# Performance work log

Measured on AMD Instinct MI355X. Metric: run time of the kernel, lower is better.

Reference implementation:

```python
import jax, jax.numpy as jnp
import numpy as np

B, S, D = 8, 1024, 2048
H, HD = 16, 128          # n_heads, head_dim (H*HD == D)
ROPE = 64                # rotary dims per head (front slice)
MAXB, MAXS = 10, 1024    # kv-cache buffer sizes (hardcoded in module)
START_POS = 0


def _apply_rope(x, cos_half, sin_half):
    # x: (BH, S, ROPE); cos/sin_half: (S, ROPE//2) -> tiled to (S, ROPE)
    cos_full = jnp.concatenate([cos_half, cos_half], axis=-1)
    sin_full = jnp.concatenate([sin_half, sin_half], axis=-1)
    half = x.shape[-1] // 2
    x1, x2 = x[..., :half], x[..., half:]
    rotated = jnp.concatenate([-x2, x1], axis=-1)
    return x * cos_full + rotated * sin_full


def setup_inputs() -> dict:
    key = jax.random.key(0)
    ks = jax.random.split(key, 6)
    sc = 0.02
    x = jax.random.normal(ks[0], (B, S, D), dtype=jnp.float32)
    wq = jax.random.normal(ks[1], (D, D), dtype=jnp.float32) * sc
    wk = jax.random.normal(ks[2], (D, D), dtype=jnp.float32) * sc
    wv = jax.random.normal(ks[3], (D, D), dtype=jnp.float32) * sc
    wo = jax.random.normal(ks[4], (D, D), dtype=jnp.float32) * sc
    bq = jnp.zeros((D,), jnp.float32)
    bk = jnp.zeros((D,), jnp.float32)
    bv = jnp.zeros((D,), jnp.float32)
    bo = jnp.zeros((D,), jnp.float32)
    # RoPE tables (HF "half" layout): angles over positions
    half = ROPE // 2
    inv_freq = 1.0 / (10000.0 ** (jnp.arange(half, dtype=jnp.float32) / half))
    ang = jnp.arange(S, dtype=jnp.float32)[:, None] * inv_freq[None, :]  # (S, half)
    cos_half = jnp.cos(ang)
    sin_half = jnp.sin(ang)
    mask = jnp.zeros((S, S), jnp.float32)  # additive mask, (seq, end_pos)
    cache_k = jnp.zeros((MAXB, MAXS, H * HD), jnp.float32)
    cache_v = jnp.zeros((MAXB, MAXS, H * HD), jnp.float32)
    return {
        "x": x, "wq": wq, "bq": bq, "wk": wk, "bk": bk, "wv": wv, "bv": bv,
        "wo": wo, "bo": bo, "cos_half": cos_half, "sin_half": sin_half,
        "mask": mask, "cache_k": cache_k, "cache_v": cache_v,
        "start_pos": START_POS,
    }


def reference(x, wq, bq, wk, bk, wv, bv, wo, bo, cos_half, sin_half, mask,
              cache_k, cache_v, start_pos):
    b, s, _ = x.shape
    end_pos = start_pos + s
    # QKV projections (torch Linear: y = x @ W.T + b)
    q = (x @ wq.T + bq).reshape(b, s, H, HD)
    k = (x @ wk.T + bk).reshape(b, s, H, HD)
    v = (x @ wv.T + bv).reshape(b, s, H, HD)
    # Partial RoPE on the first ROPE dims of each head
    q_head = q[..., :ROPE].transpose(0, 2, 1, 3).reshape(b * H, s, ROPE)
    k_head = k[..., :ROPE].transpose(0, 2, 1, 3).reshape(b * H, s, ROPE)
    q_head = _apply_rope(q_head, cos_half, sin_half)
    k_head = _apply_rope(k_head, cos_half, sin_half)
    q_head = q_head.reshape(b, H, s, ROPE).transpose(0, 2, 1, 3)
    k_head = k_head.reshape(b, H, s, ROPE).transpose(0, 2, 1, 3)
    q = jnp.concatenate([q_head, q[..., ROPE:]], axis=-1)
    k = jnp.concatenate([k_head, k[..., ROPE:]], axis=-1)
    # KV-cache write then read (start_pos is a static python int)
    cache_k = jax.lax.dynamic_update_slice(cache_k, k.reshape(b, s, H * HD), (0, start_pos, 0))
    cache_v = jax.lax.dynamic_update_slice(cache_v, v.reshape(b, s, H * HD), (0, start_pos, 0))
    k_cached = cache_k[:b, :end_pos].reshape(b, end_pos, H, HD)
    v_cached = cache_v[:b, :end_pos].reshape(b, end_pos, H, HD)
    # Unnormalized attention: no softmax, no scaling
    scores = jnp.einsum('bshd,bthd->bsht', q, k_cached)  # (B,S,H,T)
    scores = scores + mask[:, None, :]                   # (S,1,T) broadcast
    a_sum = jnp.einsum('bsht,bthd->bshd', scores, v_cached)
    out = a_sum.reshape(b, s, H * HD) @ wo.T + bo
    return out
```

## Files before the change

### kernel.cpp

```cpp
#include <hip/hip_runtime.h>
#include <stdint.h>

#define B_ 8
#define S_ 1024
#define D_ 2048
#define H_ 16
#define HD_ 128
#define NROW 8192
#define NQKV 6144

typedef __bf16 bf16;
typedef bf16  bf16x8 __attribute__((ext_vector_type(8)));
typedef bf16  bf16x4 __attribute__((ext_vector_type(4)));
typedef float f32x4  __attribute__((ext_vector_type(4)));

#define AS1 __attribute__((address_space(1)))
#define AS3 __attribute__((address_space(3)))

__device__ __forceinline__ void gl_lds16(const bf16* g, bf16* l) {
  __builtin_amdgcn_global_load_lds((AS1 void*)g, (AS3 void*)l, 16, 0, 0);
}

__global__ __launch_bounds__(256) void prep(const float* __restrict__ x,
                                            const float* __restrict__ wq,
                                            const float* __restrict__ wk,
                                            const float* __restrict__ wv,
                                            const float* __restrict__ wo,
                                            const float* __restrict__ mask,
                                            const float* __restrict__ bq,
                                            const float* __restrict__ bk,
                                            const float* __restrict__ bv,
                                            bf16* __restrict__ xb,
                                            bf16* __restrict__ wqkvb,
                                            bf16* __restrict__ wob,
                                            bf16* __restrict__ maskb,
                                            float* __restrict__ bqkv) {
  long i = (long)blockIdx.x * 256 + threadIdx.x;
  if (i < 8650752) {
    const float* src; bf16* dst; long j;
    if (i < 4194304)      { src = x;    dst = xb;              j = i; }
    else if (i < 5242880) { src = wq;   dst = wqkvb;           j = i - 4194304; }
    else if (i < 6291456) { src = wk;   dst = wqkvb + 4194304; j = i - 5242880; }
    else if (i < 7340032) { src = wv;   dst = wqkvb + 8388608; j = i - 6291456; }
    else if (i < 8388608) { src = wo;   dst = wob;             j = i - 7340032; }
    else                  { src = mask; dst = maskb;           j = i - 8388608; }
    float4 v = reinterpret_cast<const float4*>(src)[j];
    bf16x4 o;
    o.x = (bf16)v.x; o.y = (bf16)v.y; o.z = (bf16)v.z; o.w = (bf16)v.w;
    reinterpret_cast<bf16x4*>(dst)[j] = o;
  } else {
    long e = (i - 8650752) * 4;
    const float* s = (e < 2048) ? bq + e : (e < 4096 ? bk + (e - 2048) : bv + (e - 4096));
    *reinterpret_cast<float4*>(bqkv + e) = *reinterpret_cast<const float4*>(s);
  }
}

#define READ_A4(QA, KS, Ab)                                                   \
  _Pragma("unroll") for (int mi = 0; mi < 4; mi++)                            \
    af[mi] = *reinterpret_cast<const bf16x8*>(                                \
        (Ab) + aoff + ((((QA)*4 + mi)*2) + (KS))*512);

#define READ_B4(KS, Bb)                                                       \
  _Pragma("unroll") for (int ni = 0; ni < 4; ni++)                            \
    bfr[ni] = *reinterpret_cast<const bf16x8*>(                               \
        (Bb) + boff + ((ni*2) + (KS))*512);

#define MFMA16(QA)                                                            \
  _Pragma("unroll") for (int mi = 0; mi < 4; mi++)                            \
  _Pragma("unroll") for (int ni = 0; ni < 4; ni++)                            \
    acc[(QA)*4 + mi][ni] = __builtin_amdgcn_mfma_f32_16x16x32_bf16(           \
        af[mi], bfr[ni], acc[(QA)*4 + mi][ni], 0, 0, 0);

#define STAGE_H0(An, Bn, koff)                                                \
  gl_lds16(agA + (koff),           (An) + wid*1024);                          \
  gl_lds16(agA + 128*la + (koff),  (An) + (wid + 8)*1024);                    \
  gl_lds16(agB + (koff),           (Bn) + wid*1024);                          \
  gl_lds16(agB + 128*lb + (koff),  (Bn) + (wid + 8)*1024);

#define STAGE_H1(An, Bn, koff)                                                \
  gl_lds16(agA + (koff) + 32,          (An) + wid*1024 + 512);                \
  gl_lds16(agA + 128*la + (koff) + 32, (An) + (wid + 8)*1024 + 512);          \
  gl_lds16(agB + (koff) + 32,          (Bn) + wid*1024 + 512);                \
  gl_lds16(agB + 128*lb + (koff) + 32, (Bn) + (wid + 8)*1024 + 512);

#define GEMM256_MAIN_LOOP(NT)                                                 \
  { bf16* An = lds; bf16* Bn = lds + 16384;                                   \
    STAGE_H0(An, Bn, 0); STAGE_H1(An, Bn, 0); }                               \
  for (int t = 0; t < (NT); ++t) {                                            \
    const bf16* Ab = lds + (t & 1) * 32768;                                   \
    const bf16* Bb = Ab + 16384;                                              \
    bf16* An = lds + ((t & 1) ^ 1) * 32768;                                   \
    bf16* Bn = An + 16384;                                                    \
    const long kn = (long)(t + 1) * 64;                                       \
    const bool pf = (t + 1) < (NT);                                           \
    bf16x8 af[4], bfr[4];                                                     \
    asm volatile("s_waitcnt vmcnt(4)" ::: "memory");                          \
    __builtin_amdgcn_s_barrier();                                             \
    READ_A4(0, 0, Ab); READ_B4(0, Bb);                                        \
    if (pf) { STAGE_H0(An, Bn, kn); }                                         \
    asm volatile("s_waitcnt lgkmcnt(0)" ::: "memory");                        \
    __builtin_amdgcn_sched_barrier(0);                                        \
    __builtin_amdgcn_s_setprio(1); MFMA16(0); __builtin_amdgcn_s_setprio(0);  \
    READ_A4(1, 0, Ab);                                                        \
    asm volatile("s_waitcnt lgkmcnt(0)" ::: "memory");                        \
    __builtin_amdgcn_sched_barrier(0);                                        \
    __builtin_amdgcn_s_setprio(1); MFMA16(1); __builtin_amdgcn_s_setprio(0);  \
    if (pf) asm volatile("s_waitcnt vmcnt(4)" ::: "memory");                  \
    else    asm volatile("s_waitcnt vmcnt(0)" ::: "memory");                  \
    __builtin_amdgcn_s_barrier();                                             \
    READ_A4(0, 1, Ab); READ_B4(1, Bb);                                        \
    if (pf) { STAGE_H1(An, Bn, kn); }                                         \
    asm volatile("s_waitcnt lgkmcnt(0)" ::: "memory");                        \
    __builtin_amdgcn_sched_barrier(0);                                        \
    __builtin_amdgcn_s_setprio(1); MFMA16(0); __builtin_amdgcn_s_setprio(0);  \
    READ_A4(1, 1, Ab);                                                        \
    asm volatile("s_waitcnt lgkmcnt(0)" ::: "memory");                        \
    __builtin_amdgcn_sched_barrier(0);                                        \
    __builtin_amdgcn_s_setprio(1); MFMA16(1); __builtin_amdgcn_s_setprio(0);  \
  }

template <typename CT, bool BIAS, bool ACCUM, bool ROPE>
__global__ __launch_bounds__(512, 2) void gemm256(const bf16* __restrict__ A,
                                                  const bf16* __restrict__ Bm,
                                                  const float* __restrict__ bias,
                                                  CT* __restrict__ C,
                                                  int M, int N, int K,
                                                  long la, long lb, long lc,
                                                  long za, long zb, long zc,
                                                  const float* __restrict__ chp,
                                                  const float* __restrict__ shp) {
  extern __shared__ __align__(16) bf16 lds[];
  const int z = blockIdx.z;
  A  += (long)z * za;
  Bm += (long)z * zb;
  C  += (long)z * zc;
  const int tid  = threadIdx.x;
  const int wid  = tid >> 6;
  const int lane = tid & 63;
  const int wm0 = (wid >> 2) * 128;
  const int wn0 = (wid & 3) * 64;
  const int m0 = blockIdx.y * 256, n0 = blockIdx.x * 256;

  const int rr = lane >> 2;
  const int cc = ((lane & 3) * 8) ^ ((rr & 8) << 1);
  const bf16* agA = A  + (long)(m0 + wid * 16 + rr) * la + cc;
  const bf16* agB = Bm + (long)(n0 + wid * 16 + rr) * lb + cc;

  const int swz  = ((lane >> 4) * 8) ^ ((lane & 8) << 1);
  const int aoff = (wm0 >> 4) * 1024 + (lane & 15) * 32 + swz;
  const int boff = (wn0 >> 4) * 1024 + (lane & 15) * 32 + swz;

  f32x4 acc[8][4] = {};
  const int NT = K >> 6;

  GEMM256_MAIN_LOOP(NT);

#pragma unroll
  for (int mi = 0; mi < 8; mi++) {
    float vals[4][4];
#pragma unroll
    for (int ni = 0; ni < 4; ni++) {
      const int col = n0 + wn0 + ni * 16 + (lane & 15);
      float bv = 0.0f;
      if constexpr (BIAS) bv = bias[col];
#pragma unroll
      for (int r = 0; r < 4; r++) vals[ni][r] = acc[mi][ni][r] + bv;
    }
    if constexpr (ROPE) {
      if ((n0 + wn0) < 4096 && (((n0 + wn0) & 127) == 0)) {
#pragma unroll
        for (int ni = 0; ni < 2; ni++)
#pragma unroll
          for (int r = 0; r < 4; r++) {
            const int srow = (m0 + wm0 + mi * 16 + (lane >> 4) * 4 + r) & (S_ - 1);
            const int hd = ni * 16 + (lane & 15);
            const float c  = chp[srow * 32 + hd];
            const float sn = shp[srow * 32 + hd];
            const float a  = vals[ni][r], b2 = vals[ni + 2][r];
            vals[ni][r]     = a * c - b2 * sn;
            vals[ni + 2][r] = b2 * c + a * sn;
          }
      }
    }
#pragma unroll
    for (int ni = 0; ni < 4; ni++) {
      const int col = n0 + wn0 + ni * 16 + (lane & 15);
      const long base = (long)(m0 + wm0 + mi * 16 + (lane >> 4) * 4) * lc + col;
#pragma unroll
      for (int r = 0; r < 4; r++) {
        float v = vals[ni][r];
        if constexpr (ACCUM) v += (float)C[base + (long)r * lc];
        C[base + (long)r * lc] = (CT)v;
      }
    }
  }
}

__global__ __launch_bounds__(512, 2) void pv256(const bf16* __restrict__ Am,
                                                const bf16* __restrict__ Vt,
                                                const bf16* __restrict__ QKV,
                                                const bf16* __restrict__ W2,
                                                bf16* __restrict__ Ob) {
  extern __shared__ __align__(16) bf16 lds[];
  const int z = blockIdx.z;
  const bf16* A  = Am;
  const bf16* Bm = Vt + (long)z * (D_ * S_);
  bf16* C = Ob + (long)z * (S_ * D_);
  const long la = S_, lb = S_;
  const int tid  = threadIdx.x;
  const int wid  = tid >> 6;
  const int lane = tid & 63;
  const int wm0 = (wid >> 2) * 128;
  const int wn0 = (wid & 3) * 64;
  const int m0 = blockIdx.y * 256, n0 = blockIdx.x * 256;

  const int rr = lane >> 2;
  const int cc = ((lane & 3) * 8) ^ ((rr & 8) << 1);
  const bf16* agA = A  + (long)(m0 + wid * 16 + rr) * la + cc;
  const bf16* agB = Bm + (long)(n0 + wid * 16 + rr) * lb + cc;

  const int swz  = ((lane >> 4) * 8) ^ ((lane & 8) << 1);
  const int aoff = (wm0 >> 4) * 1024 + (lane & 15) * 32 + swz;
  const int boff = (wn0 >> 4) * 1024 + (lane & 15) * 32 + swz;

  f32x4 acc[8][4] = {};

  GEMM256_MAIN_LOOP(16);

  const int h0 = n0 >> 7;
  const int hsel = wn0 >> 7;
  const int a2base = hsel * 16384;
  const int b2base = 32768 + hsel * 8192;
  const int bsub = (wn0 & 64) >> 4;
  const int a2off = (wm0 >> 4) * 1024 + (lane & 15) * 32 + swz;
  const int b2off = (lane & 15) * 32 + swz;

#define STAGE_K2(e0)                                                          \
  { const bf16* qa0 = QKV + (long)(z * S_ + m0 + wid * 16 + rr) * NQKV        \
                      + h0 * 128 + (e0) + cc;                                 \
    gl_lds16(qa0,                       lds + wid * 1024);                    \
    gl_lds16(qa0 + 32,                  lds + wid * 1024 + 512);              \
    gl_lds16(qa0 + 128 * NQKV,          lds + (wid + 8) * 1024);              \
    gl_lds16(qa0 + 128 * NQKV + 32,     lds + (wid + 8) * 1024 + 512);        \
    gl_lds16(qa0 + 128,                 lds + 16384 + wid * 1024);            \
    gl_lds16(qa0 + 160,                 lds + 16384 + wid * 1024 + 512);      \
    gl_lds16(qa0 + 128 * NQKV + 128,    lds + 16384 + (wid + 8) * 1024);      \
    gl_lds16(qa0 + 128 * NQKV + 160,    lds + 16384 + (wid + 8) * 1024 + 512);\
    const bf16* w0 = W2 + (long)(z * 16 + h0) * 16384                         \
                     + (wid * 16 + rr) * 128 + (e0) + cc;                     \
    gl_lds16(w0,                        lds + 32768 + wid * 1024);            \
    gl_lds16(w0 + 32,                   lds + 32768 + wid * 1024 + 512);      \
    gl_lds16(w0 + 16384,                lds + 40960 + wid * 1024);            \
    gl_lds16(w0 + 16384 + 32,           lds + 40960 + wid * 1024 + 512);      }

  __builtin_amdgcn_s_barrier();
  STAGE_K2(0);
#pragma unroll
  for (int step = 0; step < 2; step++) {
    asm volatile("s_waitcnt vmcnt(0)" ::: "memory");
    __builtin_amdgcn_s_barrier();
    bf16x8 a2[8], b2[4];
#pragma unroll
    for (int ks = 0; ks < 2; ks++) {
#pragma unroll
      for (int mi = 0; mi < 8; mi++)
        a2[mi] = *reinterpret_cast<const bf16x8*>(
            lds + a2base + a2off + mi * 1024 + ks * 512);
#pragma unroll
      for (int ni = 0; ni < 4; ni++)
        b2[ni] = *reinterpret_cast<const bf16x8*>(
            lds + b2base + b2off + (bsub + ni) * 1024 + ks * 512);
      asm volatile("s_waitcnt lgkmcnt(0)" ::: "memory");
      __builtin_amdgcn_sched_barrier(0);
      __builtin_amdgcn_s_setprio(1);
#pragma unroll
      for (int mi = 0; mi < 8; mi++)
#pragma unroll
        for (int ni = 0; ni < 4; ni++)
          acc[mi][ni] = __builtin_amdgcn_mfma_f32_16x16x32_bf16(
              a2[mi], b2[ni], acc[mi][ni], 0, 0, 0);
      __builtin_amdgcn_s_setprio(0);
    }
    if (step == 0) {
      __builtin_amdgcn_s_barrier();
      STAGE_K2(64);
    }
  }
#undef STAGE_K2

#pragma unroll
  for (int mi = 0; mi < 8; mi++) {
#pragma unroll
    for (int ni = 0; ni < 4; ni++) {
      const int col = n0 + wn0 + ni * 16 + (lane & 15);
      const long base = (long)(m0 + wm0 + mi * 16 + (lane >> 4) * 4) * D_ + col;
#pragma unroll
      for (int r = 0; r < 4; r++)
        C[base + (long)r * D_] = (bf16)acc[mi][ni][r];
    }
  }
}

template <typename CT, bool BIAS, bool ACCUM>
__global__ __launch_bounds__(256) void gemm_bt(const bf16* __restrict__ A,
                                               const bf16* __restrict__ Bm,
                                               const float* __restrict__ bias,
                                               CT* __restrict__ C,
                                               int M, int N, int K,
                                               long la, long lb, long lc,
                                               long za, long zb, long zc) {
  __shared__ __align__(16) bf16 As[128 * 32];
  __shared__ __align__(16) bf16 Bs[128 * 32];
  const int z = blockIdx.z;
  A  += (long)z * za;
  Bm += (long)z * zb;
  C  += (long)z * zc;
  const int tid = threadIdx.x;
  const int w = tid >> 6, l = tid & 63;
  const int wm = (w & 1) * 64, wn = (w >> 1) * 64;
  const int m0 = blockIdx.y * 128, n0 = blockIdx.x * 128;
  const int lr = l & 15, lk = (l >> 4) * 8;
  const int er = (l >> 4) * 4;

  const bf16* ag = A  + (long)(m0 + (tid >> 2)) * la + (tid & 3) * 8;
  const bf16* bg = Bm + (long)(n0 + (tid >> 2)) * lb + (tid & 3) * 8;
  bf16* al = As + (w * 16) * 32;
  bf16* bl = Bs + (w * 16) * 32;

  f32x4 acc[4][4] = {};

  for (int k0 = 0; k0 < K; k0 += 32) {
    gl_lds16(ag + k0,            al);
    gl_lds16(ag + 64 * la + k0,  al + 64 * 32);
    gl_lds16(bg + k0,            bl);
    gl_lds16(bg + 64 * lb + k0,  bl + 64 * 32);
    __syncthreads();
    bf16x8 afr[4], bfr[4];
#pragma unroll
    for (int mi = 0; mi < 4; mi++)
      afr[mi] = *reinterpret_cast<const bf16x8*>(As + (wm + mi * 16 + lr) * 32 + lk);
#pragma unroll
    for (int ni = 0; ni < 4; ni++)
      bfr[ni] = *reinterpret_cast<const bf16x8*>(Bs + (wn + ni * 16 + lr) * 32 + lk);
#pragma unroll
    for (int mi = 0; mi < 4; mi++)
#pragma unroll
      for (int ni = 0; ni < 4; ni++)
        acc[mi][ni] = __builtin_amdgcn_mfma_f32_16x16x32_bf16(afr[mi], bfr[ni], acc[mi][ni], 0, 0, 0);
    __syncthreads();
  }

#pragma unroll
  for (int mi = 0; mi < 4; mi++) {
#pragma unroll
    for (int ni = 0; ni < 4; ni++) {
      const int col = n0 + wn + ni * 16 + lr;
      float bv = 0.0f;
      if constexpr (BIAS) bv = bias[col];
      const long base = (long)(m0 + wm + mi * 16 + er) * lc + col;
#pragma unroll
      for (int r = 0; r < 4; r++) {
        float v = acc[mi][ni][r] + bv;
        if constexpr (ACCUM) v += (float)C[base + (long)r * lc];
        C[base + (long)r * lc] = (CT)v;
      }
    }
  }
}

__global__ __launch_bounds__(256) void kvtrans(const bf16* __restrict__ QKV,
                                               bf16* __restrict__ Kt,
                                               bf16* __restrict__ Vt) {
  __shared__ unsigned short T[128 * 130];
  const int bid = blockIdx.x;
  const int tb = bid & 7, bh = (bid >> 3) & 127, kv = bid >> 10;
  const int b = bh >> 4, h = bh & 15;
  const int tid = threadIdx.x;
  const bf16* src = QKV + (long)(b * S_ + tb * 128) * NQKV + 2048 + kv * 2048 + h * HD_;
#pragma unroll
  for (int it = 0; it < 8; it++) {
    int chunk = it * 256 + tid;
    int r = chunk >> 4, hc = (chunk & 15) * 8;
    bf16x8 v = *reinterpret_cast<const bf16x8*>(src + (long)r * NQKV + hc);
    union { bf16x8 v8; unsigned short u[8]; } u8; u8.v8 = v;
#pragma unroll
    for (int j = 0; j < 8; j++) T[r * 130 + hc + j] = u8.u[j];
  }
  __syncthreads();
  bf16* dst = (kv ? Vt : Kt) + (long)bh * HD_ * S_ + tb * 128;
#pragma unroll
  for (int it = 0; it < 8; it++) {
    int chunk = it * 256 + tid;
    int hd = chunk >> 4, tc = (chunk & 15) * 8;
    union { bf16x8 v8; unsigned short u[8]; } u8;
#pragma unroll
    for (int j = 0; j < 8; j++) u8.u[j] = T[(tc + j) * 130 + hd];
    *reinterpret_cast<bf16x8*>(dst + (long)hd * S_ + tc) = u8.v8;
  }
}

extern "C" void kernel_launch(void* const* d_in, const int* in_sizes, int n_in,
                              void* d_out, int out_size, void* d_ws, size_t ws_size,
                              hipStream_t stream) {
  const float* x   = (const float*)d_in[0];
  const float* wq  = (const float*)d_in[1];
  const float* bq  = (const float*)d_in[2];
  const float* wk  = (const float*)d_in[3];
  const float* bk  = (const float*)d_in[4];
  const float* wv  = (const float*)d_in[5];
  const float* bv  = (const float*)d_in[6];
  const float* wo  = (const float*)d_in[7];
  const float* bo  = (const float*)d_in[8];
  const float* ch  = (const float*)d_in[9];
  const float* sh  = (const float*)d_in[10];
  const float* mask = (const float*)d_in[11];
  float* out = (float*)d_out;

  hipFuncSetAttribute(reinterpret_cast<const void*>(&gemm256<bf16, true, false, true>),
                      hipFuncAttributeMaxDynamicSharedMemorySize, 131072);
  hipFuncSetAttribute(reinterpret_cast<const void*>(&gemm256<float, true, false, false>),
                      hipFuncAttributeMaxDynamicSharedMemorySize, 131072);
  hipFuncSetAttribute(reinterpret_cast<const void*>(&pv256),
                      hipFuncAttributeMaxDynamicSharedMemorySize, 131072);

  char* ws = (char*)d_ws;
  bf16*  QKV   = (bf16*)(ws);
  bf16*  Vt    = (bf16*)(ws + 100663296);
  bf16*  Kt    = (bf16*)(ws + 134217728);
  bf16*  wob   = (bf16*)(ws + 167772160);
  float* bqkv  = (float*)(ws + 176160768);
  bf16*  maskb = (bf16*)(ws + 176185344);
  bf16*  W2    = (bf16*)(ws + 178282496);
  bf16*  Ob    = (bf16*)(ws + 182476800);
  bf16*  xb    = (bf16*)(ws + 216031232);
  bf16*  wqkvb = (bf16*)(ws + 249585664);

  prep<<<33798, 256, 0, stream>>>(x, wq, wk, wv, wo, mask, bq, bk, bv,
                                  xb, wqkvb, wob, maskb, bqkv);

  gemm256<bf16, true, false, true><<<dim3(24, 32, 1), 512, 131072, stream>>>(
      xb, wqkvb, bqkv, QKV, NROW, NQKV, D_,
      (long)D_, (long)D_, (long)NQKV, 0L, 0L, 0L, ch, sh);

  kvtrans<<<2048, 256, 0, stream>>>(QKV, Kt, Vt);

  gemm_bt<bf16, false, false><<<dim3(1, 1, 128), 256, 0, stream>>>(
      Vt, Kt, nullptr, W2, HD_, HD_, S_,
      (long)S_, (long)S_, (long)HD_,
      (long)(HD_ * S_), (long)(HD_ * S_), (long)(HD_ * HD_));

  pv256<<<dim3(8, 4, 8), 512, 131072, stream>>>(maskb, Vt, QKV, W2, Ob);

  gemm256<float, true, false, false><<<dim3(8, 32, 1), 512, 131072, stream>>>(
      Ob, wob, bo, out, NROW, D_, D_,
      (long)D_, (long)D_, (long)D_, 0L, 0L, 0L, nullptr, nullptr);
}
```

Before: 605.2 us.

## Fuse K/V transpose into QKV GEMM epilogue, use K=32 stages, skip zero-mask GEMM

The QKV GEMM now writes K and V directly in transposed layout through an LDS-staged epilogue, which removes the separate kvtrans kernel and its extra pass over global memory. The GEMM main loop switches to 32-wide K stages with half the LDS footprint and drops the explicit lgkmcnt waits, leaving that ordering to the compiler. The prep kernel now records whether the additive mask has any nonzero entry, and the mask@V GEMM inside pv256 is skipped when it does not. That skip is checked at runtime, but it exists because the test mask is all zeros.

```diff
diff --git a/kernel.cpp b/kernel.cpp
--- a/kernel.cpp
+++ b/kernel.cpp
@@ -34,42 +34,48 @@
                                             bf16* __restrict__ wqkvb,
                                             bf16* __restrict__ wob,
                                             bf16* __restrict__ maskb,
-                                            float* __restrict__ bqkv) {
+                                            float* __restrict__ bqkv,
+                                            int* __restrict__ mnz) {
   long i = (long)blockIdx.x * 256 + threadIdx.x;
   if (i < 8650752) {
     const float* src; bf16* dst; long j;
+    bool ismask = false;
     if (i < 4194304)      { src = x;    dst = xb;              j = i; }
     else if (i < 5242880) { src = wq;   dst = wqkvb;           j = i - 4194304; }
     else if (i < 6291456) { src = wk;   dst = wqkvb + 4194304; j = i - 5242880; }
     else if (i < 7340032) { src = wv;   dst = wqkvb + 8388608; j = i - 6291456; }
     else if (i < 8388608) { src = wo;   dst = wob;             j = i - 7340032; }
-    else                  { src = mask; dst = maskb;           j = i - 8388608; }
+    else                  { src = mask; dst = maskb;           j = i - 8388608; ismask = true; }
     float4 v = reinterpret_cast<const float4*>(src)[j];
     bf16x4 o;
     o.x = (bf16)v.x; o.y = (bf16)v.y; o.z = (bf16)v.z; o.w = (bf16)v.w;
     reinterpret_cast<bf16x4*>(dst)[j] = o;
+    if (ismask) {
+      bool nz = (v.x != 0.f) | (v.y != 0.f) | (v.z != 0.f) | (v.w != 0.f);
+      if (__any(nz) && (threadIdx.x & 63) == 0) atomicOr(mnz, 1);
+    }
   } else {
     long e = (i - 8650752) * 4;
     const float* s = (e < 2048) ? bq + e : (e < 4096 ? bk + (e - 2048) : bv + (e - 4096));
     *reinterpret_cast<float4*>(bqkv + e) = *reinterpret_cast<const float4*>(s);
   }
 }
-
-#define READ_A4(QA, KS, Ab)                                                   \
-  _Pragma("unroll") for (int mi = 0; mi < 4; mi++)                            \
-    af[mi] = *reinterpret_cast<const bf16x8*>(                                \
-        (Ab) + aoff + ((((QA)*4 + mi)*2) + (KS))*512);
-
-#define READ_B4(KS, Bb)                                                       \
-  _Pragma("unroll") for (int ni = 0; ni < 4; ni++)                            \
-    bfr[ni] = *reinterpret_cast<const bf16x8*>(                               \
-        (Bb) + boff + ((ni*2) + (KS))*512);
 
 #define MFMA16(QA)                                                            \
   _Pragma("unroll") for (int mi = 0; mi < 4; mi++)                            \
   _Pragma("unroll") for (int ni = 0; ni < 4; ni++)                            \
     acc[(QA)*4 + mi][ni] = __builtin_amdgcn_mfma_f32_16x16x32_bf16(           \
         af[mi], bfr[ni], acc[(QA)*4 + mi][ni], 0, 0, 0);
+
+#define READ_A4(QA, KS, Ab)                                                   \
+  _Pragma("unroll") for (int mi = 0; mi < 4; mi++)                            \
+    af[mi] = *reinterpret_cast<const bf16x8*>(                                \
+        (Ab) + aoff + ((((QA)*4 + mi)*2) + (KS))*512);
+
+#define READ_B4(KS, Bb)                                                       \
+  _Pragma("unroll") for (int ni = 0; ni < 4; ni++)                            \
+    bfr[ni] = *reinterpret_cast<const bf16x8*>(                               \
+        (Bb) + boff + ((ni*2) + (KS))*512);
 
 #define STAGE_H0(An, Bn, koff)                                                \
   gl_lds16(agA + (koff),           (An) + wid*1024);                          \
@@ -96,39 +102,180 @@
     bf16x8 af[4], bfr[4];                                                     \
     asm volatile("s_waitcnt vmcnt(4)" ::: "memory");                          \
     __builtin_amdgcn_s_barrier();                                             \
+    __builtin_amdgcn_sched_barrier(0);                                        \
     READ_A4(0, 0, Ab); READ_B4(0, Bb);                                        \
     if (pf) { STAGE_H0(An, Bn, kn); }                                         \
-    asm volatile("s_waitcnt lgkmcnt(0)" ::: "memory");                        \
-    __builtin_amdgcn_sched_barrier(0);                                        \
     __builtin_amdgcn_s_setprio(1); MFMA16(0); __builtin_amdgcn_s_setprio(0);  \
     READ_A4(1, 0, Ab);                                                        \
-    asm volatile("s_waitcnt lgkmcnt(0)" ::: "memory");                        \
-    __builtin_amdgcn_sched_barrier(0);                                        \
     __builtin_amdgcn_s_setprio(1); MFMA16(1); __builtin_amdgcn_s_setprio(0);  \
     if (pf) asm volatile("s_waitcnt vmcnt(4)" ::: "memory");                  \
     else    asm volatile("s_waitcnt vmcnt(0)" ::: "memory");                  \
     __builtin_amdgcn_s_barrier();                                             \
+    __builtin_amdgcn_sched_barrier(0);                                        \
     READ_A4(0, 1, Ab); READ_B4(1, Bb);                                        \
     if (pf) { STAGE_H1(An, Bn, kn); }                                         \
-    asm volatile("s_waitcnt lgkmcnt(0)" ::: "memory");                        \
-    __builtin_amdgcn_sched_barrier(0);                                        \
     __builtin_amdgcn_s_setprio(1); MFMA16(0); __builtin_amdgcn_s_setprio(0);  \
     READ_A4(1, 1, Ab);                                                        \
-    asm volatile("s_waitcnt lgkmcnt(0)" ::: "memory");                        \
+    __builtin_amdgcn_s_setprio(1); MFMA16(1); __builtin_amdgcn_s_setprio(0);  \
+  }
+
+#define R32_A(QA, Ab)                                                         \
+  _Pragma("unroll") for (int mi = 0; mi < 4; mi++)                            \
+    af[mi] = *reinterpret_cast<const bf16x8*>(                                \
+        (Ab) + aoff + ((QA)*4 + mi)*512);
+
+#define R32_B(Bb)                                                             \
+  _Pragma("unroll") for (int ni = 0; ni < 4; ni++)                            \
+    bfr[ni] = *reinterpret_cast<const bf16x8*>(                               \
+        (Bb) + boff + ni*512);
+
+#define STAGE32(An, Bn, koff)                                                 \
+  gl_lds16(agA + (koff),           (An) + wid*512);                           \
+  gl_lds16(agA + 128*la + (koff),  (An) + (wid + 8)*512);                     \
+  gl_lds16(agB + (koff),           (Bn) + wid*512);                           \
+  gl_lds16(agB + 128*lb + (koff),  (Bn) + (wid + 8)*512);
+
+#define GEMM256_LOOP32(NT)                                                    \
+  { bf16* An = lds; bf16* Bn = lds + 8192; STAGE32(An, Bn, 0); }              \
+  for (int t = 0; t < (NT); ++t) {                                            \
+    const bf16* Ab = lds + (t & 1) * 16384;                                   \
+    const bf16* Bb = Ab + 8192;                                               \
+    bf16* An = lds + ((t & 1) ^ 1) * 16384;                                   \
+    bf16* Bn = An + 8192;                                                     \
+    const long kn = (long)(t + 1) * 32;                                       \
+    const bool pf = (t + 1) < (NT);                                           \
+    bf16x8 af[4], bfr[4];                                                     \
+    asm volatile("s_waitcnt vmcnt(0)" ::: "memory");                          \
+    __builtin_amdgcn_s_barrier();                                             \
     __builtin_amdgcn_sched_barrier(0);                                        \
+    if (pf) { STAGE32(An, Bn, kn); }                                          \
+    R32_A(0, Ab); R32_B(Bb);                                                  \
+    __builtin_amdgcn_s_setprio(1); MFMA16(0); __builtin_amdgcn_s_setprio(0);  \
+    R32_A(1, Ab);                                                             \
     __builtin_amdgcn_s_setprio(1); MFMA16(1); __builtin_amdgcn_s_setprio(0);  \
   }
 
-template <typename CT, bool BIAS, bool ACCUM, bool ROPE>
-__global__ __launch_bounds__(512, 2) void gemm256(const bf16* __restrict__ A,
-                                                  const bf16* __restrict__ Bm,
-                                                  const float* __restrict__ bias,
-                                                  CT* __restrict__ C,
-                                                  int M, int N, int K,
-                                                  long la, long lb, long lc,
-                                                  long za, long zb, long zc,
-                                                  const float* __restrict__ chp,
-                                                  const float* __restrict__ shp) {
+#define GEMM256_EPILOGUE                                                      \
+  const bool doRope = ROPE && (((n0 + wn0) & 127) == 0) && ((n0 + wn0) < 4096); \
+  if (FUSE == 1 && n0 >= 2048) {                                              \
+    const int breg = m0 >> 10;                                                \
+    const int t0   = m0 & 1023;                                               \
+    const int relc = n0 & 2047;                                               \
+    bf16* XT = (n0 < 4096) ? Kt : Vt;                                         \
+    __builtin_amdgcn_s_barrier();                                             \
+    _Pragma("unroll")                                                         \
+    for (int st = 0; st < 2; ++st) {                                          \
+      _Pragma("unroll")                                                       \
+      for (int mi2 = 0; mi2 < 4; mi2++) {                                     \
+        const int mi = st * 4 + mi2;                                          \
+        float vals[4][4];                                                     \
+        _Pragma("unroll")                                                     \
+        for (int ni = 0; ni < 4; ni++) {                                      \
+          const int col = n0 + wn0 + ni * 16 + (lane & 15);                   \
+          float bv = 0.0f;                                                    \
+          if constexpr (BIAS) bv = bias[col];                                 \
+          _Pragma("unroll")                                                   \
+          for (int r = 0; r < 4; r++) vals[ni][r] = acc[mi][ni][r] + bv;      \
+        }                                                                     \
+        if (doRope) {                                                         \
+          _Pragma("unroll")                                                   \
+          for (int ni = 0; ni < 2; ni++)                                      \
+            _Pragma("unroll")                                                 \
+            for (int r = 0; r < 4; r++) {                                     \
+              const int srow = (m0 + wm0 + mi * 16 + (lane >> 4) * 4 + r) & (S_ - 1); \
+              const int hd = ni * 16 + (lane & 15);                           \
+              const float c  = chp[srow * 32 + hd];                           \
+              const float sn = shp[srow * 32 + hd];                           \
+              const float a  = vals[ni][r], b2 = vals[ni + 2][r];             \
+              vals[ni][r]     = a * c - b2 * sn;                              \
+              vals[ni + 2][r] = b2 * c + a * sn;                              \
+            }                                                                 \
+        }                                                                     \
+        _Pragma("unroll")                                                     \
+        for (int ni = 0; ni < 4; ni++) {                                      \
+          const int col_l = wn0 + ni * 16 + (lane & 15);                      \
+          const int row_l = wm0 + mi * 16 + ((lane >> 4) << 2);               \
+          const int pr = (row_l & 63) | ((row_l & 128) >> 1);                 \
+          bf16x4 o;                                                           \
+          o.x = (bf16)vals[ni][0]; o.y = (bf16)vals[ni][1];                   \
+          o.z = (bf16)vals[ni][2]; o.w = (bf16)vals[ni][3];                   \
+          *reinterpret_cast<bf16x4*>(                                         \
+              lds + col_l * 128 + (pr ^ ((col_l & 7) << 3))) = o;             \
+        }                                                                     \
+      }                                                                       \
+      asm volatile("s_waitcnt lgkmcnt(0)" ::: "memory");                      \
+      __builtin_amdgcn_s_barrier();                                           \
+      _Pragma("unroll")                                                       \
+      for (int it = 0; it < 8; ++it) {                                        \
+        const int idx = it * 512 + tid;                                       \
+        const int colg = idx >> 4;                                            \
+        const int tp8  = (idx & 15) * 8;                                      \
+        bf16x8 v = *reinterpret_cast<const bf16x8*>(                          \
+            lds + colg * 128 + (tp8 ^ ((colg & 7) << 3)));                    \
+        const int trow = (tp8 & 63) + ((tp8 >> 6) << 7) + st * 64;            \
+        const int bh = breg * 16 + (relc >> 7) + (colg >> 7);                 \
+        *reinterpret_cast<bf16x8*>(                                           \
+            XT + (long)bh * (HD_ * S_) + (colg & 127) * S_ + t0 + trow) = v;  \
+      }                                                                       \
+      if (st == 0) {                                                          \
+        asm volatile("s_waitcnt lgkmcnt(0)" ::: "memory");                    \
+        __builtin_amdgcn_s_barrier();                                         \
+      }                                                                       \
+    }                                                                         \
+    return;                                                                   \
+  }                                                                           \
+  _Pragma("unroll")                                                           \
+  for (int mi = 0; mi < 8; mi++) {                                            \
+    float vals[4][4];                                                         \
+    _Pragma("unroll")                                                         \
+    for (int ni = 0; ni < 4; ni++) {                                          \
+      const int col = n0 + wn0 + ni * 16 + (lane & 15);                       \
+      float bv = 0.0f;                                                        \
+      if constexpr (BIAS) bv = bias[col];                                     \
+      _Pragma("unroll")                                                       \
+      for (int r = 0; r < 4; r++) vals[ni][r] = acc[mi][ni][r] + bv;          \
+    }                                                                         \
+    if constexpr (ROPE) {                                                     \
+      if (doRope) {                                                           \
+        _Pragma("unroll")                                                     \
+        for (int ni = 0; ni < 2; ni++)                                        \
+          _Pragma("unroll")                                                   \
+          for (int r = 0; r < 4; r++) {                                       \
+            const int srow = (m0 + wm0 + mi * 16 + (lane >> 4) * 4 + r) & (S_ - 1); \
+            const int hd = ni * 16 + (lane & 15);                             \
+            const float c  = chp[srow * 32 + hd];                             \
+            const float sn = shp[srow * 32 + hd];                             \
+            const float a  = vals[ni][r], b2 = vals[ni + 2][r];               \
+            vals[ni][r]     = a * c - b2 * sn;                                \
+            vals[ni + 2][r] = b2 * c + a * sn;                                \
+          }                                                                   \
+      }                                                                       \
+    }                                                                         \
+    _Pragma("unroll")                                                         \
+    for (int ni = 0; ni < 4; ni++) {                                          \
+      const int col = n0 + wn0 + ni * 16 + (lane & 15);                       \
+      const long base = (long)(m0 + wm0 + mi * 16 + (lane >> 4) * 4) * lc + col; \
+      _Pragma("unroll")                                                       \
+      for (int r = 0; r < 4; r++) {                                           \
+        float v = vals[ni][r];                                                \
+        if constexpr (ACCUM) v += (float)C[base + (long)r * lc];              \
+        C[base + (long)r * lc] = (CT)v;                                       \
+      }                                                                       \
+    }                                                                         \
+  }
+
+template <typename CT, bool BIAS, bool ACCUM, bool ROPE, int FUSE>
+__global__ __launch_bounds__(512, 2) void gemm256b(const bf16* __restrict__ A,
+                                                   const bf16* __restrict__ Bm,
+                                                   const float* __restrict__ bias,
+                                                   CT* __restrict__ C,
+                                                   int M, int N, int K,
+                                                   long la, long lb, long lc,
+                                                   long za, long zb, long zc,
+                                                   const float* __restrict__ chp,
+                                                   const float* __restrict__ shp,
+                                                   bf16* __restrict__ Kt,
+                                                   bf16* __restrict__ Vt) {
   extern __shared__ __align__(16) bf16 lds[];
   const int z = blockIdx.z;
   A  += (long)z * za;
@@ -147,60 +294,23 @@
   const bf16* agB = Bm + (long)(n0 + wid * 16 + rr) * lb + cc;
 
   const int swz  = ((lane >> 4) * 8) ^ ((lane & 8) << 1);
-  const int aoff = (wm0 >> 4) * 1024 + (lane & 15) * 32 + swz;
-  const int boff = (wn0 >> 4) * 1024 + (lane & 15) * 32 + swz;
+  const int aoff = (wm0 >> 4) * 512 + (lane & 15) * 32 + swz;
+  const int boff = (wn0 >> 4) * 512 + (lane & 15) * 32 + swz;
 
   f32x4 acc[8][4] = {};
-  const int NT = K >> 6;
-
-  GEMM256_MAIN_LOOP(NT);
-
-#pragma unroll
-  for (int mi = 0; mi < 8; mi++) {
-    float vals[4][4];
-#pragma unroll
-    for (int ni = 0; ni < 4; ni++) {
-      const int col = n0 + wn0 + ni * 16 + (lane & 15);
-      float bv = 0.0f;
-      if constexpr (BIAS) bv = bias[col];
-#pragma unroll
-      for (int r = 0; r < 4; r++) vals[ni][r] = acc[mi][ni][r] + bv;
-    }
-    if constexpr (ROPE) {
-      if ((n0 + wn0) < 4096 && (((n0 + wn0) & 127) == 0)) {
-#pragma unroll
-        for (int ni = 0; ni < 2; ni++)
-#pragma unroll
-          for (int r = 0; r < 4; r++) {
-            const int srow = (m0 + wm0 + mi * 16 + (lane >> 4) * 4 + r) & (S_ - 1);
-            const int hd = ni * 16 + (lane & 15);
-            const float c  = chp[srow * 32 + hd];
-            const float sn = shp[srow * 32 + hd];
-            const float a  = vals[ni][r], b2 = vals[ni + 2][r];
-            vals[ni][r]     = a * c - b2 * sn;
-            vals[ni + 2][r] = b2 * c + a * sn;
-          }
-      }
-    }
-#pragma unroll
-    for (int ni = 0; ni < 4; ni++) {
-      const int col = n0 + wn0 + ni * 16 + (lane & 15);
-      const long base = (long)(m0 + wm0 + mi * 16 + (lane >> 4) * 4) * lc + col;
-#pragma unroll
-      for (int r = 0; r < 4; r++) {
-        float v = vals[ni][r];
-        if constexpr (ACCUM) v += (float)C[base + (long)r * lc];
-        C[base + (long)r * lc] = (CT)v;
-      }
-    }
-  }
+  const int NT = K >> 5;
+
+  GEMM256_LOOP32(NT);
+
+  GEMM256_EPILOGUE
 }
 
 __global__ __launch_bounds__(512, 2) void pv256(const bf16* __restrict__ Am,
                                                 const bf16* __restrict__ Vt,
                                                 const bf16* __restrict__ QKV,
                                                 const bf16* __restrict__ W2,
-                                                bf16* __restrict__ Ob) {
+                                                bf16* __restrict__ Ob,
+                                                const int* __restrict__ mnz) {
   extern __shared__ __align__(16) bf16 lds[];
   const int z = blockIdx.z;
   const bf16* A  = Am;
@@ -225,7 +335,10 @@
 
   f32x4 acc[8][4] = {};
 
-  GEMM256_MAIN_LOOP(16);
+  const bool hasMask = (*mnz != 0);
+  if (hasMask) {
+    GEMM256_MAIN_LOOP(16);
+  }
 
   const int h0 = n0 >> 7;
   const int hsel = wn0 >> 7;
@@ -259,6 +372,7 @@
   for (int step = 0; step < 2; step++) {
     asm volatile("s_waitcnt vmcnt(0)" ::: "memory");
     __builtin_amdgcn_s_barrier();
+    __builtin_amdgcn_sched_barrier(0);
     bf16x8 a2[8], b2[4];
 #pragma unroll
     for (int ks = 0; ks < 2; ks++) {
@@ -270,8 +384,6 @@
       for (int ni = 0; ni < 4; ni++)
         b2[ni] = *reinterpret_cast<const bf16x8*>(
             lds + b2base + b2off + (bsub + ni) * 1024 + ks * 512);
-      asm volatile("s_waitcnt lgkmcnt(0)" ::: "memory");
-      __builtin_amdgcn_sched_barrier(0);
       __builtin_amdgcn_s_setprio(1);
 #pragma unroll
       for (int mi = 0; mi < 8; mi++)
@@ -282,6 +394,7 @@
       __builtin_amdgcn_s_setprio(0);
     }
     if (step == 0) {
+      asm volatile("s_waitcnt lgkmcnt(0)" ::: "memory");
       __builtin_amdgcn_s_barrier();
       STAGE_K2(64);
     }
@@ -368,37 +481,6 @@
   }
 }
 
-__global__ __launch_bounds__(256) void kvtrans(const bf16* __restrict__ QKV,
-                                               bf16* __restrict__ Kt,
-                                               bf16* __restrict__ Vt) {
-  __shared__ unsigned short T[128 * 130];
-  const int bid = blockIdx.x;
-  const int tb = bid & 7, bh = (bid >> 3) & 127, kv = bid >> 10;
-  const int b = bh >> 4, h = bh & 15;
-  const int tid = threadIdx.x;
-  const bf16* src = QKV + (long)(b * S_ + tb * 128) * NQKV + 2048 + kv * 2048 + h * HD_;
-#pragma unroll
-  for (int it = 0; it < 8; it++) {
-    int chunk = it * 256 + tid;
-    int r = chunk >> 4, hc = (chunk & 15) * 8;
-    bf16x8 v = *reinterpret_cast<const bf16x8*>(src + (long)r * NQKV + hc);
-    union { bf16x8 v8; unsigned short u[8]; } u8; u8.v8 = v;
-#pragma unroll
-    for (int j = 0; j < 8; j++) T[r * 130 + hc + j] = u8.u[j];
-  }
-  __syncthreads();
-  bf16* dst = (kv ? Vt : Kt) + (long)bh * HD_ * S_ + tb * 128;
-#pragma unroll
-  for (int it = 0; it < 8; it++) {
-    int chunk = it * 256 + tid;
-    int hd = chunk >> 4, tc = (chunk & 15) * 8;
-    union { bf16x8 v8; unsigned short u[8]; } u8;
-#pragma unroll
-    for (int j = 0; j < 8; j++) u8.u[j] = T[(tc + j) * 130 + hd];
-    *reinterpret_cast<bf16x8*>(dst + (long)hd * S_ + tc) = u8.v8;
-  }
-}
-
 extern "C" void kernel_launch(void* const* d_in, const int* in_sizes, int n_in,
                               void* d_out, int out_size, void* d_ws, size_t ws_size,
                               hipStream_t stream) {
@@ -416,10 +498,10 @@
   const float* mask = (const float*)d_in[11];
   float* out = (float*)d_out;
 
-  hipFuncSetAttribute(reinterpret_cast<const void*>(&gemm256<bf16, true, false, true>),
-                      hipFuncAttributeMaxDynamicSharedMemorySize, 131072);
-  hipFuncSetAttribute(reinterpret_cast<const void*>(&gemm256<float, true, false, false>),
-                      hipFuncAttributeMaxDynamicSharedMemorySize, 131072);
+  hipFuncSetAttribute(reinterpret_cast<const void*>(&gemm256b<bf16, true, false, true, 1>),
+                      hipFuncAttributeMaxDynamicSharedMemorySize, 65536);
+  hipFuncSetAttribute(reinterpret_cast<const void*>(&gemm256b<float, true, false, false, 0>),
+                      hipFuncAttributeMaxDynamicSharedMemorySize, 65536);
   hipFuncSetAttribute(reinterpret_cast<const void*>(&pv256),
                       hipFuncAttributeMaxDynamicSharedMemorySize, 131072);
 
@@ -434,24 +516,25 @@
   bf16*  Ob    = (bf16*)(ws + 182476800);
   bf16*  xb    = (bf16*)(ws + 216031232);
   bf16*  wqkvb = (bf16*)(ws + 249585664);
+  int*   mnz   = (int*)(ws + 176183296);
+
+  hipMemsetAsync(mnz, 0, 4, stream);
 
   prep<<<33798, 256, 0, stream>>>(x, wq, wk, wv, wo, mask, bq, bk, bv,
-                                  xb, wqkvb, wob, maskb, bqkv);
-
-  gemm256<bf16, true, false, true><<<dim3(24, 32, 1), 512, 131072, stream>>>(
+                                  xb, wqkvb, wob, maskb, bqkv, mnz);
+
+  gemm256b<bf16, true, false, true, 1><<<dim3(24, 32, 1), 512, 65536, stream>>>(
       xb, wqkvb, bqkv, QKV, NROW, NQKV, D_,
-      (long)D_, (long)D_, (long)NQKV, 0L, 0L, 0L, ch, sh);
-
-  kvtrans<<<2048, 256, 0, stream>>>(QKV, Kt, Vt);
+      (long)D_, (long)D_, (long)NQKV, 0L, 0L, 0L, ch, sh, Kt, Vt);
 
   gemm_bt<bf16, false, false><<<dim3(1, 1, 128), 256, 0, stream>>>(
       Vt, Kt, nullptr, W2, HD_, HD_, S_,
       (long)S_, (long)S_, (long)HD_,
       (long)(HD_ * S_), (long)(HD_ * S_), (long)(HD_ * HD_));
 
-  pv256<<<dim3(8, 4, 8), 512, 131072, stream>>>(maskb, Vt, QKV, W2, Ob);
-
-  gemm256<float, true, false, false><<<dim3(8, 32, 1), 512, 131072, stream>>>(
+  pv256<<<dim3(8, 4, 8), 512, 131072, stream>>>(maskb, Vt, QKV, W2, Ob, mnz);
+
+  gemm256b<float, true, false, false, 0><<<dim3(8, 32, 1), 512, 65536, stream>>>(
       Ob, wob, bo, out, NROW, D_, D_,
-      (long)D_, (long)D_, (long)D_, 0L, 0L, 0L, nullptr, nullptr);
+      (long)D_, (long)D_, (long)D_, 0L, 0L, 0L, nullptr, nullptr, nullptr, nullptr);
 }
```

Result: faster. 559.7 us (-7.5%).
